# Optimization experiments

Measured on AMD Instinct MI355X. Metric: run time of the kernel, lower is better.

## Reference

```python
import jax, jax.numpy as jnp
import numpy as np

B, S, E, H = 4, 2048, 1024, 16
D = E // H  # head dim = 64


def setup_inputs() -> dict:
    key = jax.random.key(0)
    ks = jax.random.split(key, 5)
    s = 0.02
    return {
        "x": jax.random.normal(ks[0], (B, S, E), dtype=jnp.float32),
        "Wq": jax.random.normal(ks[1], (E, E), dtype=jnp.float32) * s,
        "Wk": jax.random.normal(ks[2], (E, E), dtype=jnp.float32) * s,
        "Wv": jax.random.normal(ks[3], (E, E), dtype=jnp.float32) * s,
        "Wo": jax.random.normal(ks[4], (E, E), dtype=jnp.float32) * s,
        "bo": jnp.zeros((E,), dtype=jnp.float32),
    }


def reference(x, Wq, Wk, Wv, Wo, bo):
    b, s, e = x.shape
    h, d = H, e // H
    # QKV projections -> [b, h, s, d]
    q = (x @ Wq).reshape(b, s, h, d).transpose(0, 2, 1, 3)
    k = (x @ Wk).reshape(b, s, h, d).transpose(0, 2, 1, 3)
    v = (x @ Wv).reshape(b, s, h, d).transpose(0, 2, 1, 3)
    # scores [b, h, s, s], causal mask with -inf, scaled softmax
    a = jnp.einsum('bhqd,bhkd->bhqk', q, k)
    causal = jnp.tril(jnp.ones((s, s), dtype=bool))  # True where allowed
    a = jnp.where(causal, a, -jnp.inf) / jnp.sqrt(jnp.asarray(d, x.dtype))
    a = jax.nn.softmax(a, axis=-1)
    # dropout p=0.0 (identity in eval)
    y = jnp.einsum('bhqk,bhkd->bhqd', a, v)
    y = y.transpose(0, 2, 1, 3).reshape(b, s, e)
    return y @ Wo + bo
```

## Files before the change

### kernel.cpp

```cpp
#include <hip/hip_runtime.h>

typedef __bf16 bf16x8 __attribute__((ext_vector_type(8)));
typedef float f32x4 __attribute__((ext_vector_type(4)));

#define S_LEN 2048
#define NHEAD 16
#define HDIM  64
#define EMB   1024

__device__ __forceinline__ ushort f2b(float v) {
  union { float f; unsigned u; } x; x.f = v;
  unsigned r = (x.u + 0x7fffu + ((x.u >> 16) & 1u)) >> 16;
  return (ushort)r;
}

__device__ __forceinline__ ushort f2b_trunc(float v) {
  union { float f; unsigned u; } x; x.f = v;
  return (ushort)(x.u >> 16);
}

__global__ __launch_bounds__(256) void cast_x_kernel(const float* __restrict__ x,
                                                     ushort* __restrict__ xb) {
  size_t i = ((size_t)blockIdx.x * 256 + threadIdx.x) * 4;
  float4 v = *(const float4*)(x + i);
  ushort4 o;
  o.x = f2b(v.x); o.y = f2b(v.y); o.z = f2b(v.z); o.w = f2b(v.w);
  *(ushort4*)(xb + i) = o;
}

__global__ __launch_bounds__(256) void tcast_w_kernel(const float* __restrict__ W,
                                                      ushort* __restrict__ Wt,
                                                      float scale) {
  __shared__ float t[32][33];
  int k0 = blockIdx.x * 32, n0 = blockIdx.y * 32;
  int c = threadIdx.x & 31, r0 = threadIdx.x >> 5;
#pragma unroll
  for (int i = 0; i < 4; ++i) {
    int r = r0 + i * 8;
    t[r][c] = W[(size_t)(k0 + r) * EMB + n0 + c];
  }
  __syncthreads();
#pragma unroll
  for (int i = 0; i < 4; ++i) {
    int r = r0 + i * 8;
    Wt[(size_t)(n0 + r) * EMB + k0 + c] = f2b(t[c][r] * scale);
  }
}

__global__ __launch_bounds__(256) void transpose_v_kernel(const ushort* __restrict__ V,
                                                          ushort* __restrict__ Vt) {
  __shared__ ushort t[32][33];
  int s0 = blockIdx.x * 32, d0 = blockIdx.y * 32;
  size_t base = (size_t)blockIdx.z * S_LEN * HDIM;
  int c = threadIdx.x & 31, r0 = threadIdx.x >> 5;
#pragma unroll
  for (int i = 0; i < 4; ++i) {
    int r = r0 + i * 8;
    t[r][c] = V[base + (size_t)(s0 + r) * HDIM + d0 + c];
  }
  __syncthreads();
#pragma unroll
  for (int i = 0; i < 4; ++i) {
    int r = r0 + i * 8;
    Vt[base + (size_t)(d0 + r) * S_LEN + s0 + c] = t[c][r];
  }
}

template <int EPI>
__global__ __launch_bounds__(256) void gemm_kernel(
    const ushort* __restrict__ A, const ushort* __restrict__ Bt, int K, int N,
    ushort* __restrict__ outQ, ushort* __restrict__ outK, ushort* __restrict__ outV,
    float* __restrict__ outF, const float* __restrict__ bias) {
  __shared__ ushort As[128 * 40];
  __shared__ ushort Bs[128 * 40];
  const int tid = threadIdx.x;
  const int lane = tid & 63, ln = lane & 15, quad = lane >> 4;
  const int wave = tid >> 6, wm = wave >> 1, wn = wave & 1;
  const long m0 = (long)blockIdx.x * 128, n0 = (long)blockIdx.y * 128;

  const int r1 = tid >> 2, c1 = (tid & 3) * 8;
  const ushort* Ag = A + (m0 + r1) * (long)K + c1;
  const ushort* Bg = Bt + (n0 + r1) * (long)K + c1;

  uint4 ra0 = *(const uint4*)(Ag);
  uint4 ra1 = *(const uint4*)(Ag + 64 * (long)K);
  uint4 rb0 = *(const uint4*)(Bg);
  uint4 rb1 = *(const uint4*)(Bg + 64 * (long)K);
  *(uint4*)(As + r1 * 40 + c1) = ra0;
  *(uint4*)(As + (r1 + 64) * 40 + c1) = ra1;
  *(uint4*)(Bs + r1 * 40 + c1) = rb0;
  *(uint4*)(Bs + (r1 + 64) * 40 + c1) = rb1;
  __syncthreads();

  f32x4 acc[4][4] = {};
  const int KT = K >> 5;
  for (int kt = 0; kt < KT; ++kt) {
    if (kt + 1 < KT) {
      const ushort* a2 = Ag + (kt + 1) * 32;
      const ushort* b2 = Bg + (kt + 1) * 32;
      ra0 = *(const uint4*)(a2);
      ra1 = *(const uint4*)(a2 + 64 * (long)K);
      rb0 = *(const uint4*)(b2);
      rb1 = *(const uint4*)(b2 + 64 * (long)K);
    }
    bf16x8 af[4], bf[4];
#pragma unroll
    for (int mt = 0; mt < 4; ++mt)
      af[mt] = *(const bf16x8*)(As + (wm * 64 + mt * 16 + ln) * 40 + quad * 8);
#pragma unroll
    for (int nt = 0; nt < 4; ++nt)
      bf[nt] = *(const bf16x8*)(Bs + (wn * 64 + nt * 16 + ln) * 40 + quad * 8);
#pragma unroll
    for (int mt = 0; mt < 4; ++mt)
#pragma unroll
      for (int nt = 0; nt < 4; ++nt)
        acc[mt][nt] = __builtin_amdgcn_mfma_f32_16x16x32_bf16(af[mt], bf[nt], acc[mt][nt], 0, 0, 0);
    if (kt + 1 < KT) {
      __syncthreads();
      *(uint4*)(As + r1 * 40 + c1) = ra0;
      *(uint4*)(As + (r1 + 64) * 40 + c1) = ra1;
      *(uint4*)(Bs + r1 * 40 + c1) = rb0;
      *(uint4*)(Bs + (r1 + 64) * 40 + c1) = rb1;
      __syncthreads();
    }
  }

#pragma unroll
  for (int mt = 0; mt < 4; ++mt) {
#pragma unroll
    for (int nt = 0; nt < 4; ++nt) {
#pragma unroll
      for (int r = 0; r < 4; ++r) {
        long m = m0 + wm * 64 + mt * 16 + quad * 4 + r;
        long n = n0 + wn * 64 + nt * 16 + ln;
        float v = acc[mt][nt][r];
        if (EPI == 0) {
          int sel = (int)(n >> 10);
          int nn = (int)(n & 1023);
          int h = nn >> 6, d = nn & 63;
          long b = m >> 11, s = m & 2047;
          ushort* dst = sel == 0 ? outQ : (sel == 1 ? outK : outV);
          dst[(((b * NHEAD + h) * S_LEN) + s) * HDIM + d] = f2b(v);
        } else {
          outF[m * (long)N + n] = v + bias[n];
        }
      }
    }
  }
}

__global__ __launch_bounds__(256) void attn_kernel(const ushort* __restrict__ Q,
                                                   const ushort* __restrict__ Kg,
                                                   const ushort* __restrict__ Vt,
                                                   ushort* __restrict__ Y) {
  __shared__ ushort Ks[2][64 * 72];
  __shared__ ushort Vs[2][64 * 72];
  __shared__ ushort Ps[4 * 16 * 72];
  const int tid = threadIdx.x;
  const int wave = tid >> 6, lane = tid & 63, ln = lane & 15, quad = lane >> 4;
  const int bh = blockIdx.x;
  const int qb = 15 - (int)blockIdx.y;
  const int q0 = qb * 128;
  const size_t base = (size_t)bh * S_LEN * HDIM;
  const int ntiles = 2 * qb + 2;

  bf16x8 qf[2][2];
#pragma unroll
  for (int mt = 0; mt < 2; ++mt)
#pragma unroll
    for (int ks2 = 0; ks2 < 2; ++ks2)
      qf[mt][ks2] = *(const bf16x8*)(Q + base + (size_t)(q0 + wave * 32 + mt * 16 + ln) * HDIM +
                                     ks2 * 32 + quad * 8);

  f32x4 acc[2][4] = {};
  float l_part[2][4] = {};

  const int rA = tid >> 3, cA = (tid & 7) * 8;
  const ushort* Kgb = Kg + base;
  const ushort* Vtb = Vt + base;

  uint4 rk0 = *(const uint4*)(Kgb + (size_t)rA * HDIM + cA);
  uint4 rk1 = *(const uint4*)(Kgb + (size_t)(rA + 32) * HDIM + cA);
  uint4 rv0 = *(const uint4*)(Vtb + (size_t)rA * S_LEN + cA);
  uint4 rv1 = *(const uint4*)(Vtb + (size_t)(rA + 32) * S_LEN + cA);
  *(uint4*)(&Ks[0][rA * 72 + cA]) = rk0;
  *(uint4*)(&Ks[0][(rA + 32) * 72 + cA]) = rk1;
  *(uint4*)(&Vs[0][rA * 72 + cA]) = rv0;
  *(uint4*)(&Vs[0][(rA + 32) * 72 + cA]) = rv1;
  __syncthreads();

  ushort* Pw = Ps + wave * 16 * 72;

  for (int kt = 0; kt < ntiles; ++kt) {
    const int cur = kt & 1;
    const int k0 = kt * 64;
    if (kt + 1 < ntiles) {
      const int k1 = k0 + 64;
      rk0 = *(const uint4*)(Kgb + (size_t)(k1 + rA) * HDIM + cA);
      rk1 = *(const uint4*)(Kgb + (size_t)(k1 + rA + 32) * HDIM + cA);
      rv0 = *(const uint4*)(Vtb + (size_t)rA * S_LEN + k1 + cA);
      rv1 = *(const uint4*)(Vtb + (size_t)(rA + 32) * S_LEN + k1 + cA);
    }
    const ushort* Kc = Ks[cur];
    const ushort* Vc = Vs[cur];

#pragma unroll
    for (int mt = 0; mt < 2; ++mt) {
      const int qbase = q0 + wave * 32 + mt * 16;
      if (k0 > qbase + 15) continue;

      f32x4 s[4] = {};
#pragma unroll
      for (int ks2 = 0; ks2 < 2; ++ks2) {
#pragma unroll
        for (int nt = 0; nt < 4; ++nt) {
          bf16x8 bk = *(const bf16x8*)(Kc + (nt * 16 + ln) * 72 + ks2 * 32 + quad * 8);
          s[nt] = __builtin_amdgcn_mfma_f32_16x16x32_bf16(qf[mt][ks2], bk, s[nt], 0, 0, 0);
        }
      }

      if (k0 + 63 > qbase) {
        const int rowq = qbase + quad * 4;
#pragma unroll
        for (int nt = 0; nt < 4; ++nt)
#pragma unroll
          for (int r = 0; r < 4; ++r)
            if (k0 + nt * 16 + ln > rowq + r) s[nt][r] = -3.0e38f;
      }

      asm volatile("" ::: "memory");
#pragma unroll
      for (int nt = 0; nt < 4; ++nt) {
#pragma unroll
        for (int r = 0; r < 4; ++r) {
          float p = __builtin_amdgcn_exp2f(s[nt][r]);
          l_part[mt][r] += p;
          Pw[(quad * 4 + r) * 72 + nt * 16 + ln] = f2b_trunc(p);
        }
      }
      asm volatile("" ::: "memory");

#pragma unroll
      for (int ks2 = 0; ks2 < 2; ++ks2) {
        bf16x8 ap = *(const bf16x8*)(Pw + ln * 72 + ks2 * 32 + quad * 8);
#pragma unroll
        for (int t2 = 0; t2 < 4; ++t2) {
          bf16x8 bv = *(const bf16x8*)(Vc + (t2 * 16 + ln) * 72 + ks2 * 32 + quad * 8);
          acc[mt][t2] = __builtin_amdgcn_mfma_f32_16x16x32_bf16(ap, bv, acc[mt][t2], 0, 0, 0);
        }
      }
    }

    if (kt + 1 < ntiles) {
      const int nxt = cur ^ 1;
      *(uint4*)(&Ks[nxt][rA * 72 + cA]) = rk0;
      *(uint4*)(&Ks[nxt][(rA + 32) * 72 + cA]) = rk1;
      *(uint4*)(&Vs[nxt][rA * 72 + cA]) = rv0;
      *(uint4*)(&Vs[nxt][(rA + 32) * 72 + cA]) = rv1;
    }
    __syncthreads();
  }

  const long b = bh >> 4;
  const int h = bh & 15;
#pragma unroll
  for (int mt = 0; mt < 2; ++mt) {
#pragma unroll
    for (int r = 0; r < 4; ++r) {
      float t = l_part[mt][r];
      t += __shfl_xor(t, 1);
      t += __shfl_xor(t, 2);
      t += __shfl_xor(t, 4);
      t += __shfl_xor(t, 8);
      float inv = 1.0f / t;
      const int qq = q0 + wave * 32 + mt * 16 + quad * 4 + r;
#pragma unroll
      for (int t2 = 0; t2 < 4; ++t2)
        Y[(((b * S_LEN + qq) * NHEAD) + h) * HDIM + t2 * 16 + ln] = f2b(acc[mt][t2][r] * inv);
    }
  }
}

extern "C" void kernel_launch(void* const* d_in, const int* in_sizes, int n_in,
                              void* d_out, int out_size, void* d_ws, size_t ws_size,
                              hipStream_t stream) {
  const float* x  = (const float*)d_in[0];
  const float* Wq = (const float*)d_in[1];
  const float* Wk = (const float*)d_in[2];
  const float* Wv = (const float*)d_in[3];
  const float* Wo = (const float*)d_in[4];
  const float* bo = (const float*)d_in[5];
  float* out = (float*)d_out;

  const size_t NTOK = (size_t)4 * S_LEN;
  const size_t XE = NTOK * EMB;
  ushort* ws    = (ushort*)d_ws;
  ushort* xb    = ws;
  ushort* Wtqkv = xb + XE;
  ushort* Wto   = Wtqkv + 3 * 1048576;
  ushort* Qb    = Wto + 1048576;
  ushort* Kb    = Qb + XE;
  ushort* Vb    = Kb + XE;
  ushort* Vtb   = Vb + XE;
  ushort* Yb    = xb;

  const float SCALE_Q = 1.4426950408889634f / 8.0f;

  cast_x_kernel<<<8192, 256, 0, stream>>>(x, xb);
  tcast_w_kernel<<<dim3(32, 32), 256, 0, stream>>>(Wq, Wtqkv, SCALE_Q);
  tcast_w_kernel<<<dim3(32, 32), 256, 0, stream>>>(Wk, Wtqkv + 1048576, 1.0f);
  tcast_w_kernel<<<dim3(32, 32), 256, 0, stream>>>(Wv, Wtqkv + 2097152, 1.0f);
  tcast_w_kernel<<<dim3(32, 32), 256, 0, stream>>>(Wo, Wto, 1.0f);

  gemm_kernel<0><<<dim3(64, 24), 256, 0, stream>>>(xb, Wtqkv, EMB, 3072,
                                                   Qb, Kb, Vb, nullptr, nullptr);
  transpose_v_kernel<<<dim3(64, 2, 64), 256, 0, stream>>>(Vb, Vtb);
  attn_kernel<<<dim3(64, 16), 256, 0, stream>>>(Qb, Kb, Vtb, Yb);
  gemm_kernel<1><<<dim3(64, 8), 256, 0, stream>>>(Yb, Wto, EMB, EMB,
                                                  nullptr, nullptr, nullptr, out, bo);
}
```

Measured before the change: 267.6 us.

## Use direct global-to-LDS loads with double buffering in GEMM and attention

Replaces the register-staged global loads and LDS stores in the GEMM and attention kernels with global_load_lds direct-to-LDS transfers into double buffers, dropping one barrier per GEMM iteration. The LDS layout changes to unpadded 32-wide rows, so fragment reads may hit more bank conflicts. Attention now processes both 16-row query subtiles together, sharing each K/V fragment read across two MFMAs, at the cost of coarser causal skipping. The four weight transpose-cast launches are merged into one 3D launch.

```diff
diff --git a/kernel.cpp b/kernel.cpp
--- a/kernel.cpp
+++ b/kernel.cpp
@@ -17,6 +17,13 @@
 __device__ __forceinline__ ushort f2b_trunc(float v) {
   union { float f; unsigned u; } x; x.f = v;
   return (ushort)(x.u >> 16);
+}
+
+typedef const __attribute__((address_space(1))) unsigned int* gp1_t;
+typedef __attribute__((address_space(3))) unsigned int* lp3_t;
+__device__ __forceinline__ void gld16(const ushort* g, const ushort* l) {
+  __builtin_amdgcn_global_load_lds((gp1_t)(unsigned long long)(uintptr_t)g,
+                                   (lp3_t)(unsigned int)(uintptr_t)l, 16, 0, 0);
 }
 
 __global__ __launch_bounds__(256) void cast_x_kernel(const float* __restrict__ x,
@@ -28,10 +35,20 @@
   *(ushort4*)(xb + i) = o;
 }
 
-__global__ __launch_bounds__(256) void tcast_w_kernel(const float* __restrict__ W,
-                                                      ushort* __restrict__ Wt,
-                                                      float scale) {
+__global__ __launch_bounds__(256) void tcast_w_kernel(const float* __restrict__ W0,
+                                                      const float* __restrict__ W1,
+                                                      const float* __restrict__ W2,
+                                                      const float* __restrict__ W3,
+                                                      ushort* __restrict__ Wt0,
+                                                      ushort* __restrict__ Wt1,
+                                                      ushort* __restrict__ Wt2,
+                                                      ushort* __restrict__ Wt3,
+                                                      float scale0) {
   __shared__ float t[32][33];
+  const int z = blockIdx.z;
+  const float* W = z == 0 ? W0 : (z == 1 ? W1 : (z == 2 ? W2 : W3));
+  ushort* Wt = z == 0 ? Wt0 : (z == 1 ? Wt1 : (z == 2 ? Wt2 : Wt3));
+  const float scale = z == 0 ? scale0 : 1.0f;
   int k0 = blockIdx.x * 32, n0 = blockIdx.y * 32;
   int c = threadIdx.x & 31, r0 = threadIdx.x >> 5;
 #pragma unroll
@@ -71,58 +88,57 @@
     const ushort* __restrict__ A, const ushort* __restrict__ Bt, int K, int N,
     ushort* __restrict__ outQ, ushort* __restrict__ outK, ushort* __restrict__ outV,
     float* __restrict__ outF, const float* __restrict__ bias) {
-  __shared__ ushort As[128 * 40];
-  __shared__ ushort Bs[128 * 40];
+  __shared__ ushort As[2][128 * 32];
+  __shared__ ushort Bs[2][128 * 32];
   const int tid = threadIdx.x;
   const int lane = tid & 63, ln = lane & 15, quad = lane >> 4;
   const int wave = tid >> 6, wm = wave >> 1, wn = wave & 1;
   const long m0 = (long)blockIdx.x * 128, n0 = (long)blockIdx.y * 128;
 
-  const int r1 = tid >> 2, c1 = (tid & 3) * 8;
-  const ushort* Ag = A + (m0 + r1) * (long)K + c1;
-  const ushort* Bg = Bt + (n0 + r1) * (long)K + c1;
-
-  uint4 ra0 = *(const uint4*)(Ag);
-  uint4 ra1 = *(const uint4*)(Ag + 64 * (long)K);
-  uint4 rb0 = *(const uint4*)(Bg);
-  uint4 rb1 = *(const uint4*)(Bg + 64 * (long)K);
-  *(uint4*)(As + r1 * 40 + c1) = ra0;
-  *(uint4*)(As + (r1 + 64) * 40 + c1) = ra1;
-  *(uint4*)(Bs + r1 * 40 + c1) = rb0;
-  *(uint4*)(Bs + (r1 + 64) * 40 + c1) = rb1;
-  __syncthreads();
+  const int sr = lane >> 2, sc = (lane & 3) * 8;
+  const ushort* AgL = A + (m0 + 32 * wave + sr) * (long)K + sc;
+  const ushort* BgL = Bt + (n0 + 32 * wave + sr) * (long)K + sc;
 
   f32x4 acc[4][4] = {};
   const int KT = K >> 5;
+
+  {
+    ushort* as = &As[0][32 * wave * 32];
+    ushort* bs = &Bs[0][32 * wave * 32];
+    gld16(AgL, as);
+    gld16(AgL + 16 * (long)K, as + 16 * 32);
+    gld16(BgL, bs);
+    gld16(BgL + 16 * (long)K, bs + 16 * 32);
+  }
+  __syncthreads();
+
   for (int kt = 0; kt < KT; ++kt) {
     if (kt + 1 < KT) {
-      const ushort* a2 = Ag + (kt + 1) * 32;
-      const ushort* b2 = Bg + (kt + 1) * 32;
-      ra0 = *(const uint4*)(a2);
-      ra1 = *(const uint4*)(a2 + 64 * (long)K);
-      rb0 = *(const uint4*)(b2);
-      rb1 = *(const uint4*)(b2 + 64 * (long)K);
-    }
+      const int nb = (kt + 1) & 1;
+      const ushort* a = AgL + (kt + 1) * 32;
+      const ushort* b = BgL + (kt + 1) * 32;
+      ushort* as = &As[nb][32 * wave * 32];
+      ushort* bs = &Bs[nb][32 * wave * 32];
+      gld16(a, as);
+      gld16(a + 16 * (long)K, as + 16 * 32);
+      gld16(b, bs);
+      gld16(b + 16 * (long)K, bs + 16 * 32);
+    }
+    const ushort* Ac = &As[kt & 1][0];
+    const ushort* Bc = &Bs[kt & 1][0];
     bf16x8 af[4], bf[4];
 #pragma unroll
     for (int mt = 0; mt < 4; ++mt)
-      af[mt] = *(const bf16x8*)(As + (wm * 64 + mt * 16 + ln) * 40 + quad * 8);
+      af[mt] = *(const bf16x8*)(Ac + (wm * 64 + mt * 16 + ln) * 32 + quad * 8);
 #pragma unroll
     for (int nt = 0; nt < 4; ++nt)
-      bf[nt] = *(const bf16x8*)(Bs + (wn * 64 + nt * 16 + ln) * 40 + quad * 8);
+      bf[nt] = *(const bf16x8*)(Bc + (wn * 64 + nt * 16 + ln) * 32 + quad * 8);
 #pragma unroll
     for (int mt = 0; mt < 4; ++mt)
 #pragma unroll
       for (int nt = 0; nt < 4; ++nt)
         acc[mt][nt] = __builtin_amdgcn_mfma_f32_16x16x32_bf16(af[mt], bf[nt], acc[mt][nt], 0, 0, 0);
-    if (kt + 1 < KT) {
-      __syncthreads();
-      *(uint4*)(As + r1 * 40 + c1) = ra0;
-      *(uint4*)(As + (r1 + 64) * 40 + c1) = ra1;
-      *(uint4*)(Bs + r1 * 40 + c1) = rb0;
-      *(uint4*)(Bs + (r1 + 64) * 40 + c1) = rb1;
-      __syncthreads();
-    }
+    __syncthreads();
   }
 
 #pragma unroll
@@ -153,9 +169,9 @@
                                                    const ushort* __restrict__ Kg,
                                                    const ushort* __restrict__ Vt,
                                                    ushort* __restrict__ Y) {
-  __shared__ ushort Ks[2][64 * 72];
-  __shared__ ushort Vs[2][64 * 72];
-  __shared__ ushort Ps[4 * 16 * 72];
+  __shared__ ushort Ks[2][2 * 64 * 32];
+  __shared__ ushort Vs[2][2 * 64 * 32];
+  __shared__ ushort Ps[4 * 2 * 16 * 72];
   const int tid = threadIdx.x;
   const int wave = tid >> 6, lane = tid & 63, ln = lane & 15, quad = lane >> 4;
   const int bh = blockIdx.x;
@@ -175,47 +191,49 @@
   f32x4 acc[2][4] = {};
   float l_part[2][4] = {};
 
-  const int rA = tid >> 3, cA = (tid & 7) * 8;
-  const ushort* Kgb = Kg + base;
-  const ushort* Vtb = Vt + base;
-
-  uint4 rk0 = *(const uint4*)(Kgb + (size_t)rA * HDIM + cA);
-  uint4 rk1 = *(const uint4*)(Kgb + (size_t)(rA + 32) * HDIM + cA);
-  uint4 rv0 = *(const uint4*)(Vtb + (size_t)rA * S_LEN + cA);
-  uint4 rv1 = *(const uint4*)(Vtb + (size_t)(rA + 32) * S_LEN + cA);
-  *(uint4*)(&Ks[0][rA * 72 + cA]) = rk0;
-  *(uint4*)(&Ks[0][(rA + 32) * 72 + cA]) = rk1;
-  *(uint4*)(&Vs[0][rA * 72 + cA]) = rv0;
-  *(uint4*)(&Vs[0][(rA + 32) * 72 + cA]) = rv1;
+  const int sr = lane >> 2, sc = (lane & 3) * 8;
+  const ushort* KgL = Kg + base + (size_t)(16 * wave + sr) * HDIM + sc;
+  const ushort* VgL = Vt + base + (size_t)(16 * wave + sr) * S_LEN + sc;
+
+  {
+    ushort* kb = &Ks[0][16 * wave * 32];
+    ushort* vb = &Vs[0][16 * wave * 32];
+    gld16(KgL, kb);
+    gld16(KgL + 32, kb + 2048);
+    gld16(VgL, vb);
+    gld16(VgL + 32, vb + 2048);
+  }
   __syncthreads();
 
-  ushort* Pw = Ps + wave * 16 * 72;
+  ushort* Pw0 = Ps + wave * 2304;
+  ushort* Pw1 = Pw0 + 1152;
 
   for (int kt = 0; kt < ntiles; ++kt) {
     const int cur = kt & 1;
     const int k0 = kt * 64;
     if (kt + 1 < ntiles) {
-      const int k1 = k0 + 64;
-      rk0 = *(const uint4*)(Kgb + (size_t)(k1 + rA) * HDIM + cA);
-      rk1 = *(const uint4*)(Kgb + (size_t)(k1 + rA + 32) * HDIM + cA);
-      rv0 = *(const uint4*)(Vtb + (size_t)rA * S_LEN + k1 + cA);
-      rv1 = *(const uint4*)(Vtb + (size_t)(rA + 32) * S_LEN + k1 + cA);
-    }
-    const ushort* Kc = Ks[cur];
-    const ushort* Vc = Vs[cur];
-
-#pragma unroll
-    for (int mt = 0; mt < 2; ++mt) {
-      const int qbase = q0 + wave * 32 + mt * 16;
-      if (k0 > qbase + 15) continue;
-
-      f32x4 s[4] = {};
+      const int nb = cur ^ 1;
+      const size_t k1 = (size_t)(k0 + 64);
+      ushort* kb = &Ks[nb][16 * wave * 32];
+      ushort* vb = &Vs[nb][16 * wave * 32];
+      gld16(KgL + k1 * HDIM, kb);
+      gld16(KgL + k1 * HDIM + 32, kb + 2048);
+      gld16(VgL + k1, vb);
+      gld16(VgL + k1 + 32, vb + 2048);
+    }
+    const ushort* Kc = &Ks[cur][0];
+    const ushort* Vc = &Vs[cur][0];
+    const int qbase = q0 + wave * 32;
+
+    if (k0 < qbase + 32) {
+      f32x4 s0[4] = {}, s1[4] = {};
 #pragma unroll
       for (int ks2 = 0; ks2 < 2; ++ks2) {
 #pragma unroll
         for (int nt = 0; nt < 4; ++nt) {
-          bf16x8 bk = *(const bf16x8*)(Kc + (nt * 16 + ln) * 72 + ks2 * 32 + quad * 8);
-          s[nt] = __builtin_amdgcn_mfma_f32_16x16x32_bf16(qf[mt][ks2], bk, s[nt], 0, 0, 0);
+          bf16x8 bk = *(const bf16x8*)(Kc + ks2 * 2048 + (nt * 16 + ln) * 32 + quad * 8);
+          s0[nt] = __builtin_amdgcn_mfma_f32_16x16x32_bf16(qf[0][ks2], bk, s0[nt], 0, 0, 0);
+          s1[nt] = __builtin_amdgcn_mfma_f32_16x16x32_bf16(qf[1][ks2], bk, s1[nt], 0, 0, 0);
         }
       }
 
@@ -224,8 +242,11 @@
 #pragma unroll
         for (int nt = 0; nt < 4; ++nt)
 #pragma unroll
-          for (int r = 0; r < 4; ++r)
-            if (k0 + nt * 16 + ln > rowq + r) s[nt][r] = -3.0e38f;
+          for (int r = 0; r < 4; ++r) {
+            const int key = k0 + nt * 16 + ln;
+            if (key > rowq + r) s0[nt][r] = -3.0e38f;
+            if (key > rowq + 16 + r) s1[nt][r] = -3.0e38f;
+          }
       }
 
       asm volatile("" ::: "memory");
@@ -233,30 +254,27 @@
       for (int nt = 0; nt < 4; ++nt) {
 #pragma unroll
         for (int r = 0; r < 4; ++r) {
-          float p = __builtin_amdgcn_exp2f(s[nt][r]);
-          l_part[mt][r] += p;
-          Pw[(quad * 4 + r) * 72 + nt * 16 + ln] = f2b_trunc(p);
+          float p0 = __builtin_amdgcn_exp2f(s0[nt][r]);
+          float p1 = __builtin_amdgcn_exp2f(s1[nt][r]);
+          l_part[0][r] += p0;
+          l_part[1][r] += p1;
+          Pw0[(quad * 4 + r) * 72 + nt * 16 + ln] = f2b_trunc(p0);
+          Pw1[(quad * 4 + r) * 72 + nt * 16 + ln] = f2b_trunc(p1);
         }
       }
       asm volatile("" ::: "memory");
 
 #pragma unroll
       for (int ks2 = 0; ks2 < 2; ++ks2) {
-        bf16x8 ap = *(const bf16x8*)(Pw + ln * 72 + ks2 * 32 + quad * 8);
+        bf16x8 ap0 = *(const bf16x8*)(Pw0 + ln * 72 + ks2 * 32 + quad * 8);
+        bf16x8 ap1 = *(const bf16x8*)(Pw1 + ln * 72 + ks2 * 32 + quad * 8);
 #pragma unroll
         for (int t2 = 0; t2 < 4; ++t2) {
-          bf16x8 bv = *(const bf16x8*)(Vc + (t2 * 16 + ln) * 72 + ks2 * 32 + quad * 8);
-          acc[mt][t2] = __builtin_amdgcn_mfma_f32_16x16x32_bf16(ap, bv, acc[mt][t2], 0, 0, 0);
+          bf16x8 bv = *(const bf16x8*)(Vc + ks2 * 2048 + (t2 * 16 + ln) * 32 + quad * 8);
+          acc[0][t2] = __builtin_amdgcn_mfma_f32_16x16x32_bf16(ap0, bv, acc[0][t2], 0, 0, 0);
+          acc[1][t2] = __builtin_amdgcn_mfma_f32_16x16x32_bf16(ap1, bv, acc[1][t2], 0, 0, 0);
         }
       }
-    }
-
-    if (kt + 1 < ntiles) {
-      const int nxt = cur ^ 1;
-      *(uint4*)(&Ks[nxt][rA * 72 + cA]) = rk0;
-      *(uint4*)(&Ks[nxt][(rA + 32) * 72 + cA]) = rk1;
-      *(uint4*)(&Vs[nxt][rA * 72 + cA]) = rv0;
-      *(uint4*)(&Vs[nxt][(rA + 32) * 72 + cA]) = rv1;
     }
     __syncthreads();
   }
@@ -307,10 +325,8 @@
   const float SCALE_Q = 1.4426950408889634f / 8.0f;
 
   cast_x_kernel<<<8192, 256, 0, stream>>>(x, xb);
-  tcast_w_kernel<<<dim3(32, 32), 256, 0, stream>>>(Wq, Wtqkv, SCALE_Q);
-  tcast_w_kernel<<<dim3(32, 32), 256, 0, stream>>>(Wk, Wtqkv + 1048576, 1.0f);
-  tcast_w_kernel<<<dim3(32, 32), 256, 0, stream>>>(Wv, Wtqkv + 2097152, 1.0f);
-  tcast_w_kernel<<<dim3(32, 32), 256, 0, stream>>>(Wo, Wto, 1.0f);
+  tcast_w_kernel<<<dim3(32, 32, 4), 256, 0, stream>>>(
+      Wq, Wk, Wv, Wo, Wtqkv, Wtqkv + 1048576, Wtqkv + 2097152, Wto, SCALE_Q);
 
   gemm_kernel<0><<<dim3(64, 24), 256, 0, stream>>>(xb, Wtqkv, EMB, 3072,
                                                    Qb, Kb, Vb, nullptr, nullptr);
```

After: 249.9 us. 6.6% less time.
